# Optimization experiments

Measured on AMD Instinct MI355X. Metric: run time of the kernel, lower is better.

The kernel has to match this reference:

```python
import jax, jax.numpy as jnp
import numpy as np

D_MODEL = 1024
N_HEADS = 16
D_K = D_MODEL // N_HEADS


def setup_inputs() -> dict:
    key = jax.random.key(0)
    ks = jax.random.split(key, 16)
    B, S = 2, 2048
    sc = 1.0 / np.sqrt(D_MODEL)
    inp = {
        "query": jax.random.normal(ks[0], (B, S, D_MODEL), jnp.float32),
        "key": jax.random.normal(ks[1], (B, S, D_MODEL), jnp.float32),
        "value": jax.random.normal(ks[2], (B, S, D_MODEL), jnp.float32),
        "Wq": jax.random.normal(ks[3], (D_MODEL, D_MODEL), jnp.float32) * sc,
        "bq": jnp.zeros((D_MODEL,), jnp.float32),
        "Wk": jax.random.normal(ks[4], (D_MODEL, D_MODEL), jnp.float32) * sc,
        "bk": jnp.zeros((D_MODEL,), jnp.float32),
        "Wv": jax.random.normal(ks[5], (D_MODEL, D_MODEL), jnp.float32) * sc,
        "bv": jnp.zeros((D_MODEL,), jnp.float32),
        "Wo": jax.random.normal(ks[6], (D_MODEL, D_MODEL), jnp.float32) * sc,
        "bo": jnp.zeros((D_MODEL,), jnp.float32),
        "theta": jax.random.normal(ks[7], (N_HEADS,), jnp.float32) * 0.1,
        "gate": jax.random.normal(ks[8], (D_MODEL,), jnp.float32) * 0.1,
    }
    return inp


def reference(query, key, value, Wq, bq, Wk, bk, Wv, bv, Wo, bo, theta, gate):
    B, Sq, D = query.shape
    Sk = key.shape[1]
    # linear projections (torch Linear: x @ W.T + b), split heads -> [B,H,S,d_k]
    Q = (query @ Wq.T + bq).reshape(B, Sq, N_HEADS, D_K).transpose(0, 2, 1, 3)
    K = (key @ Wk.T + bk).reshape(B, Sk, N_HEADS, D_K).transpose(0, 2, 1, 3)
    V = (value @ Wv.T + bv).reshape(B, Sk, N_HEADS, D_K).transpose(0, 2, 1, 3)

    inv_sqrt_dk = 1.0 / jnp.sqrt(jnp.float32(D_K))
    scores = jnp.einsum("bhqd,bhkd->bhqk", Q, K) * inv_sqrt_dk

    # per-head rotation of the first two feature dims of Q
    cos_t = jnp.cos(theta)[None, :, None, None]  # [1,H,1,1]
    sin_t = jnp.sin(theta)[None, :, None, None]
    q_rot = jnp.concatenate(
        [
            cos_t * Q[..., :1] - sin_t * Q[..., 1:2],
            sin_t * Q[..., :1] + cos_t * Q[..., 1:2],
            Q[..., 2:],
        ],
        axis=-1,
    )
    scores_q = jnp.einsum("bhqd,bhkd->bhqk", q_rot, K) * inv_sqrt_dk

    g_scalar = jax.nn.sigmoid(gate.mean())
    scores = g_scalar * scores_q + (1.0 - g_scalar) * scores

    attn = jax.nn.softmax(scores, axis=-1)
    out = jnp.einsum("bhqk,bhkd->bhqd", attn, V)
    out = out.transpose(0, 2, 1, 3).reshape(B, Sq, D)
    return out @ Wo.T + bo
```

## Files before the change

### kernel.cpp

```cpp
#include <hip/hip_runtime.h>


typedef __bf16 bf16;
typedef __attribute__((ext_vector_type(8))) bf16 bf16x8;
typedef __attribute__((ext_vector_type(4))) bf16 bf16x4;
typedef __attribute__((ext_vector_type(2))) bf16 bf16x2;
typedef __attribute__((ext_vector_type(4))) float f32x4;
typedef unsigned int u32;

#define D_MODEL 1024
#define NH 16
#define DKH 64
#define SEQ 2048
#define NBATCH 2

#define GLL16(g, l) __builtin_amdgcn_global_load_lds(                      \
    (const __attribute__((address_space(1))) void*)(g),                    \
    (__attribute__((address_space(3))) void*)(l), 16, 0, 0)

static __device__ __forceinline__ f32x4 mfma16(bf16x8 a, bf16x8 b, f32x4 c) {
  return __builtin_amdgcn_mfma_f32_16x16x32_bf16(a, b, c, 0, 0, 0);
}

static __device__ __forceinline__ u32 pk2(float a, float b) {
  bf16x2 v; v[0] = (bf16)a; v[1] = (bf16)b;
  return __builtin_bit_cast(u32, v);
}

__global__ __launch_bounds__(256) void wcvt(const float* __restrict__ Wq,
                                            const float* __restrict__ bq,
                                            const float* __restrict__ Wk,
                                            const float* __restrict__ Wv,
                                            const float* __restrict__ Wo,
                                            const float* __restrict__ gate,
                                            const float* __restrict__ theta,
                                            bf16* __restrict__ Wqp,
                                            bf16* __restrict__ Wkp,
                                            bf16* __restrict__ Wvp,
                                            bf16* __restrict__ Wop,
                                            float* __restrict__ bqp) {
  const int z = blockIdx.z;
  const int tid = threadIdx.x;
  if (z != 0) {
    const float* s = (z == 1) ? Wk : (z == 2) ? Wv : Wo;
    bf16* dd = (z == 1) ? Wkp : (z == 2) ? Wvp : Wop;
    const size_t i = (size_t)(blockIdx.x * 256 + tid) * 4;
    float4 v = *(const float4*)(s + i);
    bf16x4 o4; o4[0] = (bf16)v.x; o4[1] = (bf16)v.y; o4[2] = (bf16)v.z; o4[3] = (bf16)v.w;
    *(bf16x4*)(dd + i) = o4;
    return;
  }
  __shared__ float red[4];
  float ssum = 0.f;
  for (int i = tid; i < D_MODEL; i += 256) ssum += gate[i];
#pragma unroll
  for (int off = 32; off > 0; off >>= 1) ssum += __shfl_down(ssum, off);
  if ((tid & 63) == 0) red[tid >> 6] = ssum;
  __syncthreads();
  const float g = 1.f / (1.f + __expf(-(red[0] + red[1] + red[2] + red[3]) / 1024.f));

  const int t = blockIdx.x * 256 + tid;
  const int r = t >> 8;
  const int c0 = (t & 255) * 4;
  const int d = r & 63, h = r >> 6;
  float4 w = *(const float4*)(Wq + (size_t)r * D_MODEL + c0);
  float4 o;
  if (d == 0) {
    const float a = (g * cosf(theta[h]) + (1.f - g)) * 0.125f;
    const float bb = (g * sinf(theta[h])) * 0.125f;
    float4 w2 = *(const float4*)(Wq + (size_t)(r + 1) * D_MODEL + c0);
    o.x = a * w.x - bb * w2.x; o.y = a * w.y - bb * w2.y;
    o.z = a * w.z - bb * w2.z; o.w = a * w.w - bb * w2.w;
    if (c0 == 0) bqp[r] = a * bq[r] - bb * bq[r + 1];
  } else if (d == 1) {
    const float a = (g * cosf(theta[h]) + (1.f - g)) * 0.125f;
    const float bb = (g * sinf(theta[h])) * 0.125f;
    float4 w2 = *(const float4*)(Wq + (size_t)(r - 1) * D_MODEL + c0);
    o.x = bb * w2.x + a * w.x; o.y = bb * w2.y + a * w.y;
    o.z = bb * w2.z + a * w.z; o.w = bb * w2.w + a * w.w;
    if (c0 == 0) bqp[r] = bb * bq[r - 1] + a * bq[r];
  } else {
    o.x = 0.125f * w.x; o.y = 0.125f * w.y;
    o.z = 0.125f * w.z; o.w = 0.125f * w.w;
    if (c0 == 0) bqp[r] = 0.125f * bq[r];
  }
  bf16x4 ov; ov[0] = (bf16)o.x; ov[1] = (bf16)o.y; ov[2] = (bf16)o.z; ov[3] = (bf16)o.w;
  *(bf16x4*)(Wqp + (size_t)r * D_MODEL + c0) = ov;
}

__global__ __launch_bounds__(256) void cvt3(const float* __restrict__ q,
                                            const float* __restrict__ k,
                                            const float* __restrict__ v,
                                            bf16* __restrict__ xq,
                                            bf16* __restrict__ xk,
                                            bf16* __restrict__ xv) {
  const int z = blockIdx.z;
  const float* s = (z == 0) ? q : (z == 1) ? k : v;
  bf16* d = (z == 0) ? xq : (z == 1) ? xk : xv;
  const size_t i = (size_t)(blockIdx.x * 256 + threadIdx.x) * 4;
  float4 w = *(const float4*)(s + i);
  bf16x4 o; o[0] = (bf16)w.x; o[1] = (bf16)w.y; o[2] = (bf16)w.z; o[3] = (bf16)w.w;
  *(bf16x4*)(d + i) = o;
}

static __device__ __forceinline__ void gemm_bt_main(const bf16* __restrict__ A,
                                                    const bf16* __restrict__ Bt,
                                                    int tm, int tn, int K,
                                                    f32x4 acc[4][4]) {
  __shared__ bf16 lA[4096];
  __shared__ bf16 lB[4096];
  const int tid = threadIdx.x;
  const int lane = tid & 63, wv = tid >> 6;
  const int wm = wv >> 1, wn = wv & 1;
  const int l16 = lane & 15, lg = lane >> 4;

#pragma unroll
  for (int i = 0; i < 4; ++i)
#pragma unroll
    for (int j = 0; j < 4; ++j) acc[i][j] = (f32x4){0.f, 0.f, 0.f, 0.f};

  int offA[4], offB[4];
#pragma unroll
  for (int f = 0; f < 4; ++f) {
    int m = wm * 64 + f * 16 + l16;
    offA[f] = m * 32 + ((lg ^ ((m >> 1) & 3)) << 3);
    int n = wn * 64 + f * 16 + l16;
    offB[f] = n * 32 + ((lg ^ ((n >> 1) & 3)) << 3);
  }
  const int c0i = tid, c1i = 256 + tid;
  const int ma0 = c0i >> 2, sa0 = (c0i & 3) ^ ((ma0 >> 1) & 3);
  const int ma1 = c1i >> 2, sa1 = (c1i & 3) ^ ((ma1 >> 1) & 3);
  const bf16* gA0 = A + (size_t)(tm + ma0) * K + sa0 * 8;
  const bf16* gA1 = A + (size_t)(tm + ma1) * K + sa1 * 8;
  const bf16* gB0 = Bt + (size_t)(tn + ma0) * K + sa0 * 8;
  const bf16* gB1 = Bt + (size_t)(tn + ma1) * K + sa1 * 8;
  bf16* dA0 = &lA[wv * 512]; bf16* dA1 = &lA[2048 + wv * 512];
  bf16* dB0 = &lB[wv * 512]; bf16* dB1 = &lB[2048 + wv * 512];

  for (int kt = 0; kt < K; kt += 32) {
    __syncthreads();
    GLL16(gA0 + kt, dA0);
    GLL16(gA1 + kt, dA1);
    GLL16(gB0 + kt, dB0);
    GLL16(gB1 + kt, dB1);
    __syncthreads();
    bf16x8 af[4], bv[4];
#pragma unroll
    for (int f = 0; f < 4; ++f) {
      af[f] = *(const bf16x8*)&lA[offA[f]];
      bv[f] = *(const bf16x8*)&lB[offB[f]];
    }
#pragma unroll
    for (int i = 0; i < 4; ++i)
#pragma unroll
      for (int j = 0; j < 4; ++j)
        acc[i][j] = mfma16(af[i], bv[j], acc[i][j]);
  }
}

__global__ __launch_bounds__(256) void gemm_qkv(
    const bf16* __restrict__ Xq, const bf16* __restrict__ Xk, const bf16* __restrict__ Xv,
    const bf16* __restrict__ Wq, const bf16* __restrict__ Wk, const bf16* __restrict__ Wv,
    const float* __restrict__ bqp, const float* __restrict__ bk, const float* __restrict__ bv,
    bf16* __restrict__ Qp, bf16* __restrict__ Kp, bf16* __restrict__ Vt) {
  const int wgp = (blockIdx.x & 7) * 96 + (blockIdx.x >> 3);
  const int z = wgp >> 8;
  const int rem = wgp & 255;
  const int tm = (rem >> 3) * 128, tn = (rem & 7) * 128;
  const bf16* A = (z == 0) ? Xq : (z == 1) ? Xk : Xv;
  const bf16* Bt = (z == 0) ? Wq : (z == 1) ? Wk : Wv;
  const float* bias = (z == 0) ? bqp : (z == 1) ? bk : bv;
  f32x4 acc[4][4];
  gemm_bt_main(A, Bt, tm, tn, D_MODEL, acc);
  const int lane = threadIdx.x & 63, wv = threadIdx.x >> 6;
  const int wm = wv >> 1, wn = wv & 1, l16 = lane & 15, lg = lane >> 4;
  if (z < 2) {
    bf16* C = (z == 0) ? Qp : Kp;
#pragma unroll
    for (int i = 0; i < 4; ++i) {
      const int m0 = tm + wm * 64 + i * 16 + lg * 4;
#pragma unroll
      for (int j = 0; j < 4; ++j) {
        const int n = tn + wn * 64 + j * 16 + l16;
        const float bb = bias[n];
        const int h = n >> 6, d = n & 63;
#pragma unroll
        for (int r = 0; r < 4; ++r) {
          const int m = m0 + r;
          const int b = m >> 11, s = m & 2047;
          C[((size_t)(b * NH + h) * SEQ + s) * DKH + d] = (bf16)(acc[i][j][r] + bb);
        }
      }
    }
  } else {
#pragma unroll
    for (int i = 0; i < 4; ++i) {
      const int m0 = tm + wm * 64 + i * 16 + lg * 4;
      const int b = m0 >> 11, s0 = m0 & 2047;
#pragma unroll
      for (int j = 0; j < 4; ++j) {
        const int n = tn + wn * 64 + j * 16 + l16;
        const float bb = bias[n];
        const int h = n >> 6, d = n & 63;
        bf16x4 ov;
#pragma unroll
        for (int r = 0; r < 4; ++r) ov[r] = (bf16)(acc[i][j][r] + bb);
        *(bf16x4*)&Vt[((size_t)(b * NH + h) * DKH + d) * SEQ + s0] = ov;
      }
    }
  }
}

__global__ __launch_bounds__(256) void gemm_out_k(const bf16* __restrict__ A,
                                                  const bf16* __restrict__ Bt,
                                                  const float* __restrict__ bias,
                                                  float* __restrict__ C) {
  const int wgp = (blockIdx.x & 7) * 32 + (blockIdx.x >> 3);
  const int tm = (wgp >> 3) * 128, tn = (wgp & 7) * 128;
  f32x4 acc[4][4];
  gemm_bt_main(A, Bt, tm, tn, D_MODEL, acc);
  const int lane = threadIdx.x & 63, wv = threadIdx.x >> 6;
  const int wm = wv >> 1, wn = wv & 1, l16 = lane & 15, lg = lane >> 4;
#pragma unroll
  for (int i = 0; i < 4; ++i) {
    const int m0 = tm + wm * 64 + i * 16 + lg * 4;
#pragma unroll
    for (int j = 0; j < 4; ++j) {
      const int n = tn + wn * 64 + j * 16 + l16;
      const float bb = bias[n];
#pragma unroll
      for (int r = 0; r < 4; ++r)
        C[(size_t)(m0 + r) * D_MODEL + n] = acc[i][j][r] + bb;
    }
  }
}

__global__ __launch_bounds__(256, 4) void attn_kernel(const bf16* __restrict__ Qp,
                                                      const bf16* __restrict__ Kp,
                                                      const bf16* __restrict__ Vt,
                                                      bf16* __restrict__ Op) {
  __shared__ bf16 lK[4096];
  __shared__ bf16 lV[4096];
  __shared__ bf16 lP[4096];

  const int tid = threadIdx.x;
  const int lane = tid & 63, w = tid >> 6;
  const int l16 = lane & 15, lg = lane >> 4;
  const int wgp = (blockIdx.x & 7) * 128 + (blockIdx.x >> 3);
  const int bh = wgp >> 5;
  const int b = bh >> 4, h = bh & 15;
  const int q0 = (wgp & 31) * 64;
  const size_t kvb = (size_t)bh * SEQ * DKH;

  bf16x8 aq[2];
#pragma unroll
  for (int kc = 0; kc < 2; ++kc)
    aq[kc] = *(const bf16x8*)&Qp[kvb + (size_t)(q0 + w * 16 + l16) * DKH + kc * 32 + lg * 8];

  f32x4 o[4];
#pragma unroll
  for (int fn = 0; fn < 4; ++fn) o[fn] = (f32x4){0.f, 0.f, 0.f, 0.f};
  float m_run = -1e30f, l_run = 0.f;

  const int kr = tid >> 3, oct = tid & 7;
  const bf16* gK = Kp + kvb + (size_t)kr * DKH + oct * 8;
  const bf16* gV = Vt + kvb + (size_t)kr * SEQ + oct * 8;
  const int swz0 = kr * 64 + ((oct ^ (kr & 7)) << 3);
  const int swz1 = (kr + 32) * 64 + ((oct ^ (kr & 7)) << 3);

  bf16* lPw = &lP[w * 1024];
  int pwr[4];
#pragma unroll
  for (int fn = 0; fn < 4; ++fn)
    pwr[fn] = l16 * 64 + (((fn * 2 + (lg >> 1)) ^ (l16 & 7)) << 3) + ((lg & 1) << 2);
  int prd[2];
#pragma unroll
  for (int kc = 0; kc < 2; ++kc)
    prd[kc] = l16 * 64 + (((kc * 4 + lg) ^ (l16 & 7)) << 3);

  bf16x8 k0r = *(const bf16x8*)(gK);
  bf16x8 k1r = *(const bf16x8*)(gK + 32 * DKH);
  bf16x8 v0r = *(const bf16x8*)(gV);
  bf16x8 v1r = *(const bf16x8*)(gV + (size_t)32 * SEQ);

  for (int kt = 0; kt < SEQ; kt += 64) {
    __syncthreads();
    *(bf16x8*)&lK[swz0] = k0r;  *(bf16x8*)&lK[swz1] = k1r;
    *(bf16x8*)&lV[swz0] = v0r;  *(bf16x8*)&lV[swz1] = v1r;
    __syncthreads();
    if (kt + 64 < SEQ) {
      k0r = *(const bf16x8*)(gK + (size_t)(kt + 64) * DKH);
      k1r = *(const bf16x8*)(gK + (size_t)(kt + 96) * DKH);
      v0r = *(const bf16x8*)(gV + (kt + 64));
      v1r = *(const bf16x8*)(gV + (size_t)32 * SEQ + (kt + 64));
    }

    f32x4 st[4];
    __builtin_amdgcn_s_setprio(1);
#pragma unroll
    for (int fn = 0; fn < 4; ++fn) {
      const int row = fn * 16 + l16;
      bf16x8 ka = *(const bf16x8*)&lK[row * 64 + ((lg ^ (row & 7)) << 3)];
      bf16x8 kb = *(const bf16x8*)&lK[row * 64 + (((4 + lg) ^ (row & 7)) << 3)];
      f32x4 t = (f32x4){0.f, 0.f, 0.f, 0.f};
      t = mfma16(ka, aq[0], t);
      t = mfma16(kb, aq[1], t);
      st[fn] = t;
    }
    __builtin_amdgcn_s_setprio(0);

    float pm = fmaxf(fmaxf(fmaxf(st[0][0], st[0][1]), fmaxf(st[0][2], st[0][3])),
                     fmaxf(fmaxf(st[1][0], st[1][1]), fmaxf(st[1][2], st[1][3])));
    pm = fmaxf(pm, fmaxf(fmaxf(fmaxf(st[2][0], st[2][1]), fmaxf(st[2][2], st[2][3])),
                         fmaxf(fmaxf(st[3][0], st[3][1]), fmaxf(st[3][2], st[3][3]))));
    pm = fmaxf(pm, __shfl_xor(pm, 16));
    pm = fmaxf(pm, __shfl_xor(pm, 32));

    if (!__all(pm <= m_run + 8.f)) {
      const float mnew = fmaxf(m_run, pm);
      const float alpha = __expf(m_run - mnew);
      m_run = mnew;
      l_run *= alpha;
      float a4[4];
#pragma unroll
      for (int r = 0; r < 4; ++r) a4[r] = __shfl(alpha, (lg << 4) | (lg * 4 + r));
#pragma unroll
      for (int fn = 0; fn < 4; ++fn)
#pragma unroll
        for (int r = 0; r < 4; ++r) o[fn][r] *= a4[r];
    }

    float rs = 0.f;
#pragma unroll
    for (int fn = 0; fn < 4; ++fn) {
      const float p0 = __expf(st[fn][0] - m_run);
      const float p1 = __expf(st[fn][1] - m_run);
      const float p2 = __expf(st[fn][2] - m_run);
      const float p3 = __expf(st[fn][3] - m_run);
      rs += (p0 + p1) + (p2 + p3);
      uint2 pw; pw.x = pk2(p0, p1); pw.y = pk2(p2, p3);
      *(uint2*)&lPw[pwr[fn]] = pw;
    }
    rs += __shfl_xor(rs, 16);
    rs += __shfl_xor(rs, 32);
    l_run += rs;

    bf16x8 pa0 = *(const bf16x8*)&lPw[prd[0]];
    bf16x8 pa1 = *(const bf16x8*)&lPw[prd[1]];

    __builtin_amdgcn_s_setprio(1);
#pragma unroll
    for (int fn = 0; fn < 4; ++fn) {
      const int n = fn * 16 + l16;
      bf16x8 vv0 = *(const bf16x8*)&lV[n * 64 + ((lg ^ (n & 7)) << 3)];
      bf16x8 vv1 = *(const bf16x8*)&lV[n * 64 + (((4 + lg) ^ (n & 7)) << 3)];
      o[fn] = mfma16(pa0, vv0, o[fn]);
      o[fn] = mfma16(pa1, vv1, o[fn]);
    }
    __builtin_amdgcn_s_setprio(0);
  }

  float linv[4];
#pragma unroll
  for (int r = 0; r < 4; ++r)
    linv[r] = 1.f / __shfl(l_run, (lg << 4) | (lg * 4 + r));
#pragma unroll
  for (int r = 0; r < 4; ++r) {
    const int q = q0 + w * 16 + lg * 4 + r;
#pragma unroll
    for (int fn = 0; fn < 4; ++fn) {
      const int d = fn * 16 + l16;
      Op[((size_t)(b * SEQ + q)) * D_MODEL + h * DKH + d] = (bf16)(o[fn][r] * linv[r]);
    }
  }
}

extern "C" void kernel_launch(void* const* d_in, const int* in_sizes, int n_in,
                              void* d_out, int out_size, void* d_ws, size_t ws_size,
                              hipStream_t stream) {
  (void)in_sizes; (void)n_in; (void)out_size; (void)ws_size;
  const float* query = (const float*)d_in[0];
  const float* key   = (const float*)d_in[1];
  const float* value = (const float*)d_in[2];
  const float* Wq    = (const float*)d_in[3];
  const float* bq    = (const float*)d_in[4];
  const float* Wk    = (const float*)d_in[5];
  const float* bk    = (const float*)d_in[6];
  const float* Wv    = (const float*)d_in[7];
  const float* bv    = (const float*)d_in[8];
  const float* Wo    = (const float*)d_in[9];
  const float* bo    = (const float*)d_in[10];
  const float* theta = (const float*)d_in[11];
  const float* gate  = (const float*)d_in[12];

  float* bqp = (float*)d_ws;
  bf16* wb = (bf16*)((char*)d_ws + 8192);
  bf16* Xq  = wb;
  bf16* Xk  = Xq + 4194304;
  bf16* Xv  = Xk + 4194304;
  bf16* Wqp = Xv + 4194304;
  bf16* Wkp = Wqp + 1048576;
  bf16* Wvp = Wkp + 1048576;
  bf16* Wop = Wvp + 1048576;
  bf16* Qp  = Wop + 1048576;
  bf16* Kp  = Qp + 4194304;
  bf16* Vt  = Kp + 4194304;
  bf16* Op  = Vt + 4194304;

  wcvt<<<dim3(1024, 1, 4), 256, 0, stream>>>(Wq, bq, Wk, Wv, Wo, gate, theta,
                                             Wqp, Wkp, Wvp, Wop, bqp);
  cvt3<<<dim3(4096, 1, 3), 256, 0, stream>>>(query, key, value, Xq, Xk, Xv);
  gemm_qkv<<<768, 256, 0, stream>>>(Xq, Xk, Xv, Wqp, Wkp, Wvp,
                                    bqp, bk, bv, Qp, Kp, Vt);
  attn_kernel<<<1024, 256, 0, stream>>>(Qp, Kp, Vt, Op);
  gemm_out_k<<<256, 256, 0, stream>>>(Op, Wop, bo, (float*)d_out);
}
```

Baseline: 149.7 us.

## Merge conversion kernels, deepen GEMM k-tile, keep P in registers, use exp2

The two fp32-to-bf16 conversion kernels become one launch. The shared GEMM main loop now stages 64-wide k-tiles with an 8-way XOR swizzle, which halves the number of barrier pairs per tile. In attention, Q is prescaled by log2(e)/8 so softmax can use exp2. The P probabilities are fed straight from registers into 16x16x16 MFMA instructions, so the LDS round-trip for P is gone. The cost is larger GEMM LDS use (32KB), which may lower occupancy, and a dependence on the 16x16x16bf16_1k builtin being available.

Result: faster. 142.4 us (-4.9%).

```diff
diff --git a/kernel.cpp b/kernel.cpp
--- a/kernel.cpp
+++ b/kernel.cpp
@@ -6,13 +6,13 @@
 typedef __attribute__((ext_vector_type(4))) bf16 bf16x4;
 typedef __attribute__((ext_vector_type(2))) bf16 bf16x2;
 typedef __attribute__((ext_vector_type(4))) float f32x4;
+typedef __attribute__((ext_vector_type(4))) short s16x4;
 typedef unsigned int u32;
 
 #define D_MODEL 1024
 #define NH 16
 #define DKH 64
 #define SEQ 2048
-#define NBATCH 2
 
 #define GLL16(g, l) __builtin_amdgcn_global_load_lds(                      \
     (const __attribute__((address_space(1))) void*)(g),                    \
@@ -22,29 +22,67 @@
   return __builtin_amdgcn_mfma_f32_16x16x32_bf16(a, b, c, 0, 0, 0);
 }
 
+#if __has_builtin(__builtin_amdgcn_mfma_f32_16x16x16bf16_1k)
+#define HAVE_MFMA_K16 1
+static __device__ __forceinline__ f32x4 mfma16k16(s16x4 a, s16x4 b, f32x4 c) {
+  return __builtin_amdgcn_mfma_f32_16x16x16bf16_1k(a, b, c, 0, 0, 0);
+}
+#else
+#define HAVE_MFMA_K16 0
+#endif
+
 static __device__ __forceinline__ u32 pk2(float a, float b) {
   bf16x2 v; v[0] = (bf16)a; v[1] = (bf16)b;
   return __builtin_bit_cast(u32, v);
 }
 
-__global__ __launch_bounds__(256) void wcvt(const float* __restrict__ Wq,
+static __device__ __forceinline__ float fexp2(float x) {
+#if __has_builtin(__builtin_amdgcn_exp2f)
+  return __builtin_amdgcn_exp2f(x);
+#else
+  return exp2f(x);
+#endif
+}
+
+#define CQK 0.1803368801111244f
+
+__global__ __launch_bounds__(256) void prep(const float* __restrict__ query,
+                                            const float* __restrict__ key,
+                                            const float* __restrict__ value,
+                                            const float* __restrict__ Wq,
                                             const float* __restrict__ bq,
                                             const float* __restrict__ Wk,
                                             const float* __restrict__ Wv,
                                             const float* __restrict__ Wo,
                                             const float* __restrict__ gate,
                                             const float* __restrict__ theta,
+                                            bf16* __restrict__ Xq,
+                                            bf16* __restrict__ Xk,
+                                            bf16* __restrict__ Xv,
                                             bf16* __restrict__ Wqp,
                                             bf16* __restrict__ Wkp,
                                             bf16* __restrict__ Wvp,
                                             bf16* __restrict__ Wop,
                                             float* __restrict__ bqp) {
-  const int z = blockIdx.z;
+  const int id = blockIdx.x;
   const int tid = threadIdx.x;
-  if (z != 0) {
-    const float* s = (z == 1) ? Wk : (z == 2) ? Wv : Wo;
-    bf16* dd = (z == 1) ? Wkp : (z == 2) ? Wvp : Wop;
-    const size_t i = (size_t)(blockIdx.x * 256 + tid) * 4;
+  if (id >= 4096) {
+    const int rem = id - 4096;
+    const int iz = rem >> 12;
+    const int ib = rem & 4095;
+    const float* s = (iz == 0) ? query : (iz == 1) ? key : value;
+    bf16* d = (iz == 0) ? Xq : (iz == 1) ? Xk : Xv;
+    const size_t i = (size_t)(ib * 256 + tid) * 4;
+    float4 w = *(const float4*)(s + i);
+    bf16x4 o; o[0] = (bf16)w.x; o[1] = (bf16)w.y; o[2] = (bf16)w.z; o[3] = (bf16)w.w;
+    *(bf16x4*)(d + i) = o;
+    return;
+  }
+  const int wz = id >> 10, wb = id & 1023;
+  if (wz != 0) {
+    const float* s = (wz == 1) ? Wk : (wz == 2) ? Wv : Wo;
+    bf16* dd = (wz == 1) ? Wkp : (wz == 2) ? Wvp : Wop;
+    const size_t i = (size_t)(wb * 256 + tid) * 4;
     float4 v = *(const float4*)(s + i);
     bf16x4 o4; o4[0] = (bf16)v.x; o4[1] = (bf16)v.y; o4[2] = (bf16)v.z; o4[3] = (bf16)v.w;
     *(bf16x4*)(dd + i) = o4;
@@ -59,56 +97,41 @@
   __syncthreads();
   const float g = 1.f / (1.f + __expf(-(red[0] + red[1] + red[2] + red[3]) / 1024.f));
 
-  const int t = blockIdx.x * 256 + tid;
+  const int t = wb * 256 + tid;
   const int r = t >> 8;
   const int c0 = (t & 255) * 4;
   const int d = r & 63, h = r >> 6;
   float4 w = *(const float4*)(Wq + (size_t)r * D_MODEL + c0);
   float4 o;
   if (d == 0) {
-    const float a = (g * cosf(theta[h]) + (1.f - g)) * 0.125f;
-    const float bb = (g * sinf(theta[h])) * 0.125f;
+    const float a = (g * cosf(theta[h]) + (1.f - g)) * CQK;
+    const float bb = (g * sinf(theta[h])) * CQK;
     float4 w2 = *(const float4*)(Wq + (size_t)(r + 1) * D_MODEL + c0);
     o.x = a * w.x - bb * w2.x; o.y = a * w.y - bb * w2.y;
     o.z = a * w.z - bb * w2.z; o.w = a * w.w - bb * w2.w;
     if (c0 == 0) bqp[r] = a * bq[r] - bb * bq[r + 1];
   } else if (d == 1) {
-    const float a = (g * cosf(theta[h]) + (1.f - g)) * 0.125f;
-    const float bb = (g * sinf(theta[h])) * 0.125f;
+    const float a = (g * cosf(theta[h]) + (1.f - g)) * CQK;
+    const float bb = (g * sinf(theta[h])) * CQK;
     float4 w2 = *(const float4*)(Wq + (size_t)(r - 1) * D_MODEL + c0);
     o.x = bb * w2.x + a * w.x; o.y = bb * w2.y + a * w.y;
     o.z = bb * w2.z + a * w.z; o.w = bb * w2.w + a * w.w;
     if (c0 == 0) bqp[r] = bb * bq[r - 1] + a * bq[r];
   } else {
-    o.x = 0.125f * w.x; o.y = 0.125f * w.y;
-    o.z = 0.125f * w.z; o.w = 0.125f * w.w;
-    if (c0 == 0) bqp[r] = 0.125f * bq[r];
+    o.x = CQK * w.x; o.y = CQK * w.y;
+    o.z = CQK * w.z; o.w = CQK * w.w;
+    if (c0 == 0) bqp[r] = CQK * bq[r];
   }
   bf16x4 ov; ov[0] = (bf16)o.x; ov[1] = (bf16)o.y; ov[2] = (bf16)o.z; ov[3] = (bf16)o.w;
   *(bf16x4*)(Wqp + (size_t)r * D_MODEL + c0) = ov;
-}
-
-__global__ __launch_bounds__(256) void cvt3(const float* __restrict__ q,
-                                            const float* __restrict__ k,
-                                            const float* __restrict__ v,
-                                            bf16* __restrict__ xq,
-                                            bf16* __restrict__ xk,
-                                            bf16* __restrict__ xv) {
-  const int z = blockIdx.z;
-  const float* s = (z == 0) ? q : (z == 1) ? k : v;
-  bf16* d = (z == 0) ? xq : (z == 1) ? xk : xv;
-  const size_t i = (size_t)(blockIdx.x * 256 + threadIdx.x) * 4;
-  float4 w = *(const float4*)(s + i);
-  bf16x4 o; o[0] = (bf16)w.x; o[1] = (bf16)w.y; o[2] = (bf16)w.z; o[3] = (bf16)w.w;
-  *(bf16x4*)(d + i) = o;
 }
 
 static __device__ __forceinline__ void gemm_bt_main(const bf16* __restrict__ A,
                                                     const bf16* __restrict__ Bt,
                                                     int tm, int tn, int K,
                                                     f32x4 acc[4][4]) {
-  __shared__ bf16 lA[4096];
-  __shared__ bf16 lB[4096];
+  __shared__ bf16 lA[8192];
+  __shared__ bf16 lB[8192];
   const int tid = threadIdx.x;
   const int lane = tid & 63, wv = tid >> 6;
   const int wm = wv >> 1, wn = wv & 1;
@@ -119,42 +142,49 @@
 #pragma unroll
     for (int j = 0; j < 4; ++j) acc[i][j] = (f32x4){0.f, 0.f, 0.f, 0.f};
 
-  int offA[4], offB[4];
-#pragma unroll
-  for (int f = 0; f < 4; ++f) {
-    int m = wm * 64 + f * 16 + l16;
-    offA[f] = m * 32 + ((lg ^ ((m >> 1) & 3)) << 3);
-    int n = wn * 64 + f * 16 + l16;
-    offB[f] = n * 32 + ((lg ^ ((n >> 1) & 3)) << 3);
-  }
-  const int c0i = tid, c1i = 256 + tid;
-  const int ma0 = c0i >> 2, sa0 = (c0i & 3) ^ ((ma0 >> 1) & 3);
-  const int ma1 = c1i >> 2, sa1 = (c1i & 3) ^ ((ma1 >> 1) & 3);
-  const bf16* gA0 = A + (size_t)(tm + ma0) * K + sa0 * 8;
-  const bf16* gA1 = A + (size_t)(tm + ma1) * K + sa1 * 8;
-  const bf16* gB0 = Bt + (size_t)(tn + ma0) * K + sa0 * 8;
-  const bf16* gB1 = Bt + (size_t)(tn + ma1) * K + sa1 * 8;
-  bf16* dA0 = &lA[wv * 512]; bf16* dA1 = &lA[2048 + wv * 512];
-  bf16* dB0 = &lB[wv * 512]; bf16* dB1 = &lB[2048 + wv * 512];
-
-  for (int kt = 0; kt < K; kt += 32) {
+  int offA[4][2], offB[4][2];
+#pragma unroll
+  for (int f = 0; f < 4; ++f)
+#pragma unroll
+    for (int kc = 0; kc < 2; ++kc) {
+      const int m = wm * 64 + f * 16 + l16;
+      offA[f][kc] = m * 64 + (((kc * 4 + lg) ^ (m & 7)) << 3);
+      const int n = wn * 64 + f * 16 + l16;
+      offB[f][kc] = n * 64 + (((kc * 4 + lg) ^ (n & 7)) << 3);
+    }
+
+  const int rowb = tid >> 3, oct = tid & 7;
+  const int soct = oct ^ (rowb & 7);
+  const bf16* gA[4];
+  const bf16* gB[4];
+#pragma unroll
+  for (int rd = 0; rd < 4; ++rd) {
+    gA[rd] = A + (size_t)(tm + rd * 32 + rowb) * K + soct * 8;
+    gB[rd] = Bt + (size_t)(tn + rd * 32 + rowb) * K + soct * 8;
+  }
+
+  for (int kt = 0; kt < K; kt += 64) {
     __syncthreads();
-    GLL16(gA0 + kt, dA0);
-    GLL16(gA1 + kt, dA1);
-    GLL16(gB0 + kt, dB0);
-    GLL16(gB1 + kt, dB1);
+#pragma unroll
+    for (int rd = 0; rd < 4; ++rd) {
+      GLL16(gA[rd] + kt, &lA[rd * 2048 + wv * 512]);
+      GLL16(gB[rd] + kt, &lB[rd * 2048 + wv * 512]);
+    }
     __syncthreads();
-    bf16x8 af[4], bv[4];
-#pragma unroll
-    for (int f = 0; f < 4; ++f) {
-      af[f] = *(const bf16x8*)&lA[offA[f]];
-      bv[f] = *(const bf16x8*)&lB[offB[f]];
-    }
-#pragma unroll
-    for (int i = 0; i < 4; ++i)
-#pragma unroll
-      for (int j = 0; j < 4; ++j)
-        acc[i][j] = mfma16(af[i], bv[j], acc[i][j]);
+#pragma unroll
+    for (int kc = 0; kc < 2; ++kc) {
+      bf16x8 af[4], bv[4];
+#pragma unroll
+      for (int f = 0; f < 4; ++f) {
+        af[f] = *(const bf16x8*)&lA[offA[f][kc]];
+        bv[f] = *(const bf16x8*)&lB[offB[f][kc]];
+      }
+#pragma unroll
+      for (int i = 0; i < 4; ++i)
+#pragma unroll
+        for (int j = 0; j < 4; ++j)
+          acc[i][j] = mfma16(af[i], bv[j], acc[i][j]);
+    }
   }
 }
 
@@ -241,7 +271,9 @@
                                                       bf16* __restrict__ Op) {
   __shared__ bf16 lK[4096];
   __shared__ bf16 lV[4096];
+#if !HAVE_MFMA_K16
   __shared__ bf16 lP[4096];
+#endif
 
   const int tid = threadIdx.x;
   const int lane = tid & 63, w = tid >> 6;
@@ -268,6 +300,7 @@
   const int swz0 = kr * 64 + ((oct ^ (kr & 7)) << 3);
   const int swz1 = (kr + 32) * 64 + ((oct ^ (kr & 7)) << 3);
 
+#if !HAVE_MFMA_K16
   bf16* lPw = &lP[w * 1024];
   int pwr[4];
 #pragma unroll
@@ -277,6 +310,7 @@
 #pragma unroll
   for (int kc = 0; kc < 2; ++kc)
     prd[kc] = l16 * 64 + (((kc * 4 + lg) ^ (l16 & 7)) << 3);
+#endif
 
   bf16x8 k0r = *(const bf16x8*)(gK);
   bf16x8 k1r = *(const bf16x8*)(gK + 32 * DKH);
@@ -318,7 +352,7 @@
 
     if (!__all(pm <= m_run + 8.f)) {
       const float mnew = fmaxf(m_run, pm);
-      const float alpha = __expf(m_run - mnew);
+      const float alpha = fexp2(m_run - mnew);
       m_run = mnew;
       l_run *= alpha;
       float a4[4];
@@ -331,24 +365,45 @@
     }
 
     float rs = 0.f;
+#if HAVE_MFMA_K16
+    s16x4 paf[4];
+#endif
 #pragma unroll
     for (int fn = 0; fn < 4; ++fn) {
-      const float p0 = __expf(st[fn][0] - m_run);
-      const float p1 = __expf(st[fn][1] - m_run);
-      const float p2 = __expf(st[fn][2] - m_run);
-      const float p3 = __expf(st[fn][3] - m_run);
+      const float p0 = fexp2(st[fn][0] - m_run);
+      const float p1 = fexp2(st[fn][1] - m_run);
+      const float p2 = fexp2(st[fn][2] - m_run);
+      const float p3 = fexp2(st[fn][3] - m_run);
       rs += (p0 + p1) + (p2 + p3);
       uint2 pw; pw.x = pk2(p0, p1); pw.y = pk2(p2, p3);
+#if HAVE_MFMA_K16
+      paf[fn] = __builtin_bit_cast(s16x4, pw);
+#else
       *(uint2*)&lPw[pwr[fn]] = pw;
+#endif
     }
     rs += __shfl_xor(rs, 16);
     rs += __shfl_xor(rs, 32);
     l_run += rs;
 
+    __builtin_amdgcn_s_setprio(1);
+#if HAVE_MFMA_K16
+#pragma unroll
+    for (int dt = 0; dt < 4; ++dt) {
+      const int d = dt * 16 + l16;
+      const int drow = d * 64, dx = d & 7;
+      f32x4 acc = o[dt];
+#pragma unroll
+      for (int fn = 0; fn < 4; ++fn) {
+        const int o2 = (fn * 2 + (lg >> 1)) ^ dx;
+        s16x4 vf = *(const s16x4*)&lV[drow + (o2 << 3) + ((lg & 1) << 2)];
+        acc = mfma16k16(paf[fn], vf, acc);
+      }
+      o[dt] = acc;
+    }
+#else
     bf16x8 pa0 = *(const bf16x8*)&lPw[prd[0]];
     bf16x8 pa1 = *(const bf16x8*)&lPw[prd[1]];
-
-    __builtin_amdgcn_s_setprio(1);
 #pragma unroll
     for (int fn = 0; fn < 4; ++fn) {
       const int n = fn * 16 + l16;
@@ -357,6 +412,7 @@
       o[fn] = mfma16(pa0, vv0, o[fn]);
       o[fn] = mfma16(pa1, vv1, o[fn]);
     }
+#endif
     __builtin_amdgcn_s_setprio(0);
   }
 
@@ -407,9 +463,9 @@
   bf16* Vt  = Kp + 4194304;
   bf16* Op  = Vt + 4194304;
 
-  wcvt<<<dim3(1024, 1, 4), 256, 0, stream>>>(Wq, bq, Wk, Wv, Wo, gate, theta,
-                                             Wqp, Wkp, Wvp, Wop, bqp);
-  cvt3<<<dim3(4096, 1, 3), 256, 0, stream>>>(query, key, value, Xq, Xk, Xv);
+  prep<<<16384, 256, 0, stream>>>(query, key, value, Wq, bq, Wk, Wv, Wo,
+                                  gate, theta, Xq, Xk, Xv,
+                                  Wqp, Wkp, Wvp, Wop, bqp);
   gemm_qkv<<<768, 256, 0, stream>>>(Xq, Xk, Xv, Wqp, Wkp, Wvp,
                                     bqp, bk, bv, Qp, Kp, Vt);
   attn_kernel<<<1024, 256, 0, stream>>>(Qp, Kp, Vt, Op);
```
